# Performance work log

Hardware: AMD Instinct MI355X
Metric: run time of the kernel (lower is better)

The kernel has to match this reference:

```python
import jax, jax.numpy as jnp
import numpy as np

D_MODEL, NUM_HEADS, D_FF = 1024, 16, 4096
HEAD_DIM = D_MODEL // NUM_HEADS
EPS = 1e-5


def _layernorm(x, g, b):
    m = jnp.mean(x, axis=-1, keepdims=True)
    v = jnp.mean((x - m) ** 2, axis=-1, keepdims=True)
    return (x - m) * jax.lax.rsqrt(v + EPS) * g + b


def setup_inputs() -> dict:
    key = jax.random.key(0)
    ks = jax.random.split(key, 16)
    N, S = 4, 2048
    x = jax.random.normal(ks[0], (N, S, D_MODEL), dtype=jnp.float32)
    # mask broadcastable against energy of shape (N, S, H, H) -- see notes: code
    # computes per-position head-vs-head attention, not SxS attention.
    mask = jax.random.randint(ks[1], (N, 1, 1, NUM_HEADS), 0, 2, dtype=jnp.int32)
    s = 0.02
    return {
        "x": x,
        "Wqkv": jax.random.normal(ks[2], (D_MODEL, 3 * D_MODEL), dtype=jnp.float32) * s,
        "bqkv": jnp.zeros((3 * D_MODEL,), jnp.float32),
        "Wo": jax.random.normal(ks[3], (D_MODEL, D_MODEL), dtype=jnp.float32) * s,
        "bo": jnp.zeros((D_MODEL,), jnp.float32),
        "g1": jnp.ones((D_MODEL,), jnp.float32),
        "beta1": jnp.zeros((D_MODEL,), jnp.float32),
        "W1": jax.random.normal(ks[4], (D_MODEL, D_FF), dtype=jnp.float32) * s,
        "bf1": jnp.zeros((D_FF,), jnp.float32),
        "W2": jax.random.normal(ks[5], (D_FF, D_MODEL), dtype=jnp.float32) * s,
        "bf2": jnpp if False else jnp.zeros((D_MODEL,), jnp.float32),
        "g2": jnp.ones((D_MODEL,), jnp.float32),
        "beta2": jnp.zeros((D_MODEL,), jnp.float32),
        "mask": mask,
    }


def reference(x, Wqkv, bqkv, Wo, bo, g1, beta1, W1, bf1, W2, bf2, g2, beta2, mask):
    N, S, D = x.shape
    H, hd = NUM_HEADS, HEAD_DIM
    # fused QKV projection
    qkv = (x @ Wqkv + bqkv).reshape(N, S, 3, H, hd).transpose(2, 0, 3, 1, 4)
    q, k, v = qkv[0], qkv[1], qkv[2]  # each (N, H, S, hd)
    # faithful to torch einsum 'nqhd,nkhd->nhqk' on (N,H,S,hd) operands:
    # energy[n,s,i,j] = sum_d q[n,i,s,d] * k[n,j,s,d]  -> (N, S, H, H)
    energy = jnp.einsum('nise,njse->nsij', q, k)
    energy = jnp.where(mask == 0, jnp.float32(-1e20), energy)
    attn = jax.nn.softmax(energy / np.sqrt(hd).astype(np.float32), axis=3)
    # torch einsum 'nhql,nlhd->nqhd': out[n,i,s,d] = sum_l attn[n,s,i,l]*v[n,l,s,d]
    out = jnp.einsum('nsil,nlse->nise', attn, v)  # (N, H, S, hd)
    out = out.reshape(N, S, D)  # row-major flatten, exactly as torch .reshape
    attn_out = out @ Wo + bo
    h = _layernorm(attn_out + x, g1, beta1)
    ff = jax.nn.relu(h @ W1 + bf1) @ W2 + bf2  # dropout = identity (eval)
    return _layernorm(ff + h, g2, beta2)
```

## Files before the change

### kernel.cpp

```cpp
#include <hip/hip_runtime.h>
#include <cstdint>
#include <cstddef>


using f32x4  = __attribute__((ext_vector_type(4))) float;
using bf16x8 = __attribute__((ext_vector_type(8))) __bf16;

__device__ __forceinline__ unsigned short f2b(float f) {
  union { float f; uint32_t u; } v; v.f = f;
  uint32_t r = v.u + 0x7FFFu + ((v.u >> 16) & 1u);
  return (unsigned short)(r >> 16);
}
__device__ __forceinline__ float b2f(unsigned short u) {
  union { uint32_t u; float f; } v; v.u = ((uint32_t)u) << 16;
  return v.f;
}

__device__ __forceinline__ void gload_lds16(const unsigned short* g,
                                            unsigned short* l) {
  __builtin_amdgcn_global_load_lds(
      (const __attribute__((address_space(1))) unsigned int*)g,
      (__attribute__((address_space(3))) unsigned int*)l, 16, 0, 0);
}

#define MEMBAR() asm volatile("" ::: "memory")
__device__ __forceinline__ void barrier_raw() {
  MEMBAR();
  __builtin_amdgcn_s_barrier();
  MEMBAR();
}
template <int N>
__device__ __forceinline__ void vmwait() {
  if constexpr (N == 6)      asm volatile("s_waitcnt vmcnt(6)" ::: "memory");
  else if constexpr (N == 5) asm volatile("s_waitcnt vmcnt(5)" ::: "memory");
  else                       asm volatile("s_waitcnt vmcnt(0)" ::: "memory");
}

__global__ __launch_bounds__(256) void transpose_cvt_kernel(
    const float* __restrict__ W, unsigned short* __restrict__ WT, int K, int N) {
  __shared__ float tile[32][33];
  const int j0 = blockIdx.x * 32, k0 = blockIdx.y * 32;
  const int tx = threadIdx.x, ty = threadIdx.y;
#pragma unroll
  for (int i = 0; i < 4; ++i)
    tile[ty + 8 * i][tx] = W[(size_t)(k0 + ty + 8 * i) * N + j0 + tx];
  __syncthreads();
#pragma unroll
  for (int i = 0; i < 4; ++i)
    WT[(size_t)(j0 + ty + 8 * i) * K + k0 + tx] = f2b(tile[tx][ty + 8 * i]);
}

__global__ __launch_bounds__(256) void cvt_bf16_kernel(
    const float* __restrict__ in, unsigned short* __restrict__ out, int n4) {
  for (int i = blockIdx.x * blockDim.x + threadIdx.x; i < n4;
       i += gridDim.x * blockDim.x) {
    float4 v = ((const float4*)in)[i];
    uint32_t lo = (uint32_t)f2b(v.x) | ((uint32_t)f2b(v.y) << 16);
    uint32_t hi = (uint32_t)f2b(v.z) | ((uint32_t)f2b(v.w) << 16);
    ((uint2*)out)[i] = make_uint2(lo, hi);
  }
}

template <int BN, bool OUTB, bool RELU>
__global__ __launch_bounds__(512, 2) void gemm8p_kernel(
    const unsigned short* __restrict__ A, const unsigned short* __restrict__ B,
    const float* __restrict__ bias, void* __restrict__ C, int M, int N, int K,
    int nbn) {
  constexpr int NF   = BN / 128;
  constexpr int WN   = BN / 8;
  constexpr int BH   = BN / 2;
  constexpr int BIS  = BN / 128;
  constexpr int INF  = 4 + BN / 128;
  constexpr int ASTR = (256 + BN) * 64;

  __shared__ unsigned short lds[2 * ASTR];

  const int tid  = threadIdx.x;
  const int lane = tid & 63, wave = tid >> 6;
  const int wm = wave >> 2, wn = wave & 3;
  const int lr = lane & 15, lk = lane >> 4;
  const int x7 = lr & 7;

  const int nwg = gridDim.x, cpx = nwg >> 3, id = blockIdx.x;
  const int wg = (id & 7) * cpx + (id >> 3);
  const int bn = wg % nbn, bm = wg / nbn;

  const unsigned short* Ab = A + (size_t)bm * 256 * K;
  const unsigned short* Bb = B + (size_t)bn * BN * K;

  const int srow = tid >> 3;
  const int scol = ((tid & 7) ^ (srow & 7)) * 8;
  const int ldst = wave * 8 * 64;

  const int NT = K >> 6;

  f32x4 acc[8][2 * NF] = {};
  bf16x8 aF[4][2], b0F[NF][2], b1F[NF][2];

  auto stA = [&](int t, int h, int b) {
#pragma unroll
    for (int i = 0; i < 2; ++i)
      gload_lds16(Ab + (size_t)(h * 128 + i * 64 + srow) * K + t * 64 + scol,
                  &lds[b * ASTR + (h * 128 + i * 64) * 64 + ldst]);
  };
  auto stB = [&](int t, int h, int b) {
#pragma unroll
    for (int i = 0; i < BIS; ++i)
      gload_lds16(Bb + (size_t)(h * BH + i * 64 + srow) * K + t * 64 + scol,
                  &lds[b * ASTR + 256 * 64 + (h * BH + i * 64) * 64 + ldst]);
  };
  auto rdA = [&](int b, int mh) {
#pragma unroll
    for (int mi = 0; mi < 4; ++mi) {
      int r = mh * 128 + wm * 64 + mi * 16 + lr;
#pragma unroll
      for (int kk = 0; kk < 2; ++kk)
        aF[mi][kk] = *(const bf16x8*)
            &lds[b * ASTR + r * 64 + ((kk * 4 + lk) ^ x7) * 8];
    }
  };
  auto rdB = [&](int b, int nh, bf16x8 (&bF)[NF][2]) {
#pragma unroll
    for (int ni = 0; ni < NF; ++ni) {
      int r = nh * BH + wn * WN + ni * 16 + lr;
#pragma unroll
      for (int kk = 0; kk < 2; ++kk)
        bF[ni][kk] = *(const bf16x8*)
            &lds[b * ASTR + 256 * 64 + r * 64 + ((kk * 4 + lk) ^ x7) * 8];
    }
  };
  auto mmQ = [&](bf16x8 (&bF)[NF][2], int mh, int nh) {
    __builtin_amdgcn_s_setprio(1);
#pragma unroll
    for (int mi = 0; mi < 4; ++mi)
#pragma unroll
      for (int ni = 0; ni < NF; ++ni)
#pragma unroll
        for (int kk = 0; kk < 2; ++kk)
          acc[mh * 4 + mi][nh * NF + ni] = __builtin_amdgcn_mfma_f32_16x16x32_bf16(
              aF[mi][kk], bF[ni][kk], acc[mh * 4 + mi][nh * NF + ni], 0, 0, 0);
    __builtin_amdgcn_s_setprio(0);
  };

  stA(0, 0, 0); stB(0, 0, 0); stA(0, 1, 0); stB(0, 1, 0);
  stA(1, 0, 1); stB(1, 0, 1); stA(1, 1, 1);
  vmwait<INF>();
  barrier_raw();

  for (int t = 0; t < NT; ++t) {
    const int b = t & 1;
    const bool s1 = (t + 1 < NT), s2 = (t + 2 < NT);
    rdA(b, 0);
    rdB(b, 0, b0F);
    if (s1) stB(t + 1, 1, b ^ 1);
    barrier_raw();
    mmQ(b0F, 0, 0);
    barrier_raw();
    rdB(b, 1, b1F);
    if (s2) stA(t + 2, 0, b);
    barrier_raw();
    mmQ(b1F, 0, 1);
    barrier_raw();
    rdA(b, 1);
    if (s2) stB(t + 2, 0, b);
    barrier_raw();
    mmQ(b1F, 1, 1);
    barrier_raw();
    if (s2) {
      stA(t + 2, 1, b);
      vmwait<INF>();
    } else if (s1) {
      vmwait<0>();
    }
    barrier_raw();
    mmQ(b0F, 1, 0);
    barrier_raw();
  }

  const int orow0 = bm * 256 + wm * 64;
  const int ocol0 = bn * BN + wn * WN;
#pragma unroll
  for (int mh = 0; mh < 2; ++mh)
#pragma unroll
    for (int nh = 0; nh < 2; ++nh)
#pragma unroll
      for (int ni = 0; ni < NF; ++ni) {
        int col = ocol0 + nh * BH + ni * 16 + lr;
        float bv = bias[col];
#pragma unroll
        for (int mi = 0; mi < 4; ++mi)
#pragma unroll
          for (int r = 0; r < 4; ++r) {
            int row = orow0 + mh * 128 + mi * 16 + lk * 4 + r;
            float val = acc[mh * 4 + mi][nh * NF + ni][r] + bv;
            if (RELU) val = fmaxf(val, 0.f);
            if (OUTB)
              ((unsigned short*)C)[(size_t)row * N + col] = f2b(val);
            else
              ((float*)C)[(size_t)row * N + col] = val;
          }
      }
}

__global__ __launch_bounds__(256) void attn_kernel(
    const unsigned short* __restrict__ qkv, const int* __restrict__ mask,
    unsigned short* __restrict__ outb) {
  __shared__ float sq[16][68], sk[16][68], sv[16][68];
  __shared__ float sp[16][17];
  const int pos = blockIdx.x;
  const int n = pos >> 11, s = pos & 2047;
  const int tid = threadIdx.x;
  const unsigned short* row = qkv + (size_t)pos * 3072;
#pragma unroll
  for (int it = 0; it < 3; ++it) {
    uint2 raw = *(const uint2*)(row + it * 1024 + tid * 4);
    float f0 = b2f((unsigned short)(raw.x & 0xffffu));
    float f1 = b2f((unsigned short)(raw.x >> 16));
    float f2 = b2f((unsigned short)(raw.y & 0xffffu));
    float f3 = b2f((unsigned short)(raw.y >> 16));
    float(*dst)[68] = (it == 0) ? sq : (it == 1) ? sk : sv;
    int r = tid >> 4, d = (tid & 15) * 4;
    dst[r][d] = f0; dst[r][d + 1] = f1; dst[r][d + 2] = f2; dst[r][d + 3] = f3;
  }
  __syncthreads();
  {
    const int i = tid >> 4, j = tid & 15;
    float e = 0.f;
#pragma unroll
    for (int d = 0; d < 64; d += 4) {
      float4 qa = *(const float4*)&sq[i][d];
      float4 kb = *(const float4*)&sk[j][d];
      e += qa.x * kb.x + qa.y * kb.y + qa.z * kb.z + qa.w * kb.w;
    }
    if (mask[n * 16 + j] == 0) e = -1e20f;
    e *= 0.125f;
    float mx = e;
#pragma unroll
    for (int o = 8; o > 0; o >>= 1) mx = fmaxf(mx, __shfl_xor(mx, o, 16));
    float pe = __expf(e - mx);
    float sm = pe;
#pragma unroll
    for (int o = 8; o > 0; o >>= 1) sm += __shfl_xor(sm, o, 16);
    sp[i][j] = pe / sm;
  }
  __syncthreads();
  {
    const int w = tid >> 6, d = tid & 63;
    float o0 = 0, o1 = 0, o2 = 0, o3 = 0;
#pragma unroll
    for (int l = 0; l < 16; ++l) {
      float vv = sv[l][d];
      o0 += sp[w][l] * vv;      o1 += sp[w + 4][l] * vv;
      o2 += sp[w + 8][l] * vv;  o3 += sp[w + 12][l] * vv;
    }
    outb[(((size_t)n * 16 + w     ) * 2048 + s) * 64 + d] = f2b(o0);
    outb[(((size_t)n * 16 + w + 4 ) * 2048 + s) * 64 + d] = f2b(o1);
    outb[(((size_t)n * 16 + w + 8 ) * 2048 + s) * 64 + d] = f2b(o2);
    outb[(((size_t)n * 16 + w + 12) * 2048 + s) * 64 + d] = f2b(o3);
  }
}

__global__ __launch_bounds__(256) void ln_kernel(
    const float* __restrict__ A, const float* __restrict__ R,
    const float* __restrict__ g, const float* __restrict__ be,
    float* __restrict__ outf, unsigned short* __restrict__ outb) {
  const int row = blockIdx.x, tid = threadIdx.x;
  const size_t base = (size_t)row * 1024 + tid * 4;
  float4 a = *(const float4*)(A + base);
  float4 r = *(const float4*)(R + base);
  float x0 = a.x + r.x, x1 = a.y + r.y, x2 = a.z + r.z, x3 = a.w + r.w;
  float s = x0 + x1 + x2 + x3;
#pragma unroll
  for (int o = 32; o > 0; o >>= 1) s += __shfl_xor(s, o);
  __shared__ float red[4];
  const int lane = tid & 63, wv = tid >> 6;
  if (lane == 0) red[wv] = s;
  __syncthreads();
  float mean = (red[0] + red[1] + red[2] + red[3]) * (1.f / 1024.f);
  float d0 = x0 - mean, d1 = x1 - mean, d2 = x2 - mean, d3 = x3 - mean;
  float q = d0 * d0 + d1 * d1 + d2 * d2 + d3 * d3;
#pragma unroll
  for (int o = 32; o > 0; o >>= 1) q += __shfl_xor(q, o);
  __syncthreads();
  if (lane == 0) red[wv] = q;
  __syncthreads();
  float var = (red[0] + red[1] + red[2] + red[3]) * (1.f / 1024.f);
  float rs = rsqrtf(var + 1e-5f);
  const int col = tid * 4;
  float4 gv = *(const float4*)(g + col);
  float4 bv = *(const float4*)(be + col);
  float y0 = d0 * rs * gv.x + bv.x;
  float y1 = d1 * rs * gv.y + bv.y;
  float y2 = d2 * rs * gv.z + bv.z;
  float y3 = d3 * rs * gv.w + bv.w;
  *(float4*)(outf + base) = make_float4(y0, y1, y2, y3);
  if (outb) {
    uint32_t lo = (uint32_t)f2b(y0) | ((uint32_t)f2b(y1) << 16);
    uint32_t hi = (uint32_t)f2b(y2) | ((uint32_t)f2b(y3) << 16);
    *(uint2*)(outb + base) = make_uint2(lo, hi);
  }
}

extern "C" void kernel_launch(void* const* d_in, const int* in_sizes, int n_in,
                              void* d_out, int out_size, void* d_ws,
                              size_t ws_size, hipStream_t stream) {
  (void)in_sizes; (void)n_in; (void)out_size; (void)ws_size;
  const float* x     = (const float*)d_in[0];
  const float* Wqkv  = (const float*)d_in[1];
  const float* bqkv  = (const float*)d_in[2];
  const float* Wo    = (const float*)d_in[3];
  const float* bo    = (const float*)d_in[4];
  const float* g1    = (const float*)d_in[5];
  const float* beta1 = (const float*)d_in[6];
  const float* W1    = (const float*)d_in[7];
  const float* bf1   = (const float*)d_in[8];
  const float* W2    = (const float*)d_in[9];
  const float* bf2   = (const float*)d_in[10];
  const float* g2    = (const float*)d_in[11];
  const float* beta2 = (const float*)d_in[12];
  const int*   mask  = (const int*)d_in[13];
  float* out = (float*)d_out;

  char* ws = (char*)d_ws;
  unsigned short* WqkvT = (unsigned short*)(ws + 0);
  unsigned short* WoT   = (unsigned short*)(ws + 6291456);
  unsigned short* W1T   = (unsigned short*)(ws + 8388608);
  unsigned short* W2T   = (unsigned short*)(ws + 16777216);
  unsigned short* xb    = (unsigned short*)(ws + 25165824);
  float*          h_f   = (float*)(ws + 41943040);
  unsigned short* h_b   = (unsigned short*)(ws + 75497472);
  float*          ao2   = (float*)(ws + 92274688);
  unsigned short* qkvb  = (unsigned short*)(ws + 125829120);
  unsigned short* aob   = (unsigned short*)(ws + 176160768);
  unsigned short* ff1   = qkvb;
  float*          ff2   = ao2;

  transpose_cvt_kernel<<<dim3(96, 32),  dim3(32, 8), 0, stream>>>(Wqkv, WqkvT, 1024, 3072);
  transpose_cvt_kernel<<<dim3(32, 32),  dim3(32, 8), 0, stream>>>(Wo,   WoT,   1024, 1024);
  transpose_cvt_kernel<<<dim3(128, 32), dim3(32, 8), 0, stream>>>(W1,   W1T,   1024, 4096);
  transpose_cvt_kernel<<<dim3(32, 128), dim3(32, 8), 0, stream>>>(W2,   W2T,   4096, 1024);
  cvt_bf16_kernel<<<2048, 256, 0, stream>>>(x, xb, 8192 * 1024 / 4);

  gemm8p_kernel<256, true, false><<<dim3(32 * 12), 512, 0, stream>>>(xb, WqkvT, bqkv, qkvb, 8192, 3072, 1024, 12);
  attn_kernel<<<8192, 256, 0, stream>>>(qkvb, mask, aob);
  gemm8p_kernel<128, false, false><<<dim3(32 * 8), 512, 0, stream>>>(aob, WoT, bo, ao2, 8192, 1024, 1024, 8);
  ln_kernel<<<8192, 256, 0, stream>>>(ao2, x, g1, beta1, h_f, h_b);
  gemm8p_kernel<256, true, true><<<dim3(32 * 16), 512, 0, stream>>>(h_b, W1T, bf1, ff1, 8192, 4096, 1024, 16);
  gemm8p_kernel<128, false, false><<<dim3(32 * 8), 512, 0, stream>>>(ff1, W2T, bf2, ff2, 8192, 1024, 4096, 8);
  ln_kernel<<<8192, 256, 0, stream>>>(ff2, h_f, g2, beta2, out, nullptr);
}
```

Measured before the change: 329.8 us.

## Use split-K with wider tiles for FFN2 GEMM and merge partials in LayerNorm

Measured after the change: 329.8 us. No clear change (+0.0%).

```diff
diff --git a/kernel.cpp b/kernel.cpp
--- a/kernel.cpp
+++ b/kernel.cpp
@@ -61,11 +61,11 @@
   }
 }
 
-template <int BN, bool OUTB, bool RELU>
+template <int BN, bool SPLITK, bool OUTB, bool RELU>
 __global__ __launch_bounds__(512, 2) void gemm8p_kernel(
     const unsigned short* __restrict__ A, const unsigned short* __restrict__ B,
-    const float* __restrict__ bias, void* __restrict__ C, int M, int N, int K,
-    int nbn) {
+    const float* __restrict__ bias, void* __restrict__ C,
+    unsigned short* __restrict__ C2, int M, int N, int Ks, int Kd, int nbn) {
   constexpr int NF   = BN / 128;
   constexpr int WN   = BN / 8;
   constexpr int BH   = BN / 2;
@@ -83,16 +83,18 @@
 
   const int nwg = gridDim.x, cpx = nwg >> 3, id = blockIdx.x;
   const int wg = (id & 7) * cpx + (id >> 3);
-  const int bn = wg % nbn, bm = wg / nbn;
-
-  const unsigned short* Ab = A + (size_t)bm * 256 * K;
-  const unsigned short* Bb = B + (size_t)bn * BN * K;
+  int bm, bn, sk;
+  if (SPLITK) { bm = wg >> 3; bn = (wg & 7) >> 1; sk = wg & 1; }
+  else        { bm = wg / nbn; bn = wg % nbn; sk = 0; }
+
+  const unsigned short* Ab = A + (size_t)bm * 256 * Ks + (size_t)sk * Kd;
+  const unsigned short* Bb = B + (size_t)bn * BN * Ks + (size_t)sk * Kd;
 
   const int srow = tid >> 3;
   const int scol = ((tid & 7) ^ (srow & 7)) * 8;
   const int ldst = wave * 8 * 64;
 
-  const int NT = K >> 6;
+  const int NT = Kd >> 6;
 
   f32x4 acc[8][2 * NF] = {};
   bf16x8 aF[4][2], b0F[NF][2], b1F[NF][2];
@@ -100,13 +102,13 @@
   auto stA = [&](int t, int h, int b) {
 #pragma unroll
     for (int i = 0; i < 2; ++i)
-      gload_lds16(Ab + (size_t)(h * 128 + i * 64 + srow) * K + t * 64 + scol,
+      gload_lds16(Ab + (size_t)(h * 128 + i * 64 + srow) * Ks + t * 64 + scol,
                   &lds[b * ASTR + (h * 128 + i * 64) * 64 + ldst]);
   };
   auto stB = [&](int t, int h, int b) {
 #pragma unroll
     for (int i = 0; i < BIS; ++i)
-      gload_lds16(Bb + (size_t)(h * BH + i * 64 + srow) * K + t * 64 + scol,
+      gload_lds16(Bb + (size_t)(h * BH + i * 64 + srow) * Ks + t * 64 + scol,
                   &lds[b * ASTR + 256 * 64 + (h * BH + i * 64) * 64 + ldst]);
   };
   auto rdA = [&](int b, int mh) {
@@ -192,12 +194,20 @@
 #pragma unroll
           for (int r = 0; r < 4; ++r) {
             int row = orow0 + mh * 128 + mi * 16 + lk * 4 + r;
-            float val = acc[mh * 4 + mi][nh * NF + ni][r] + bv;
-            if (RELU) val = fmaxf(val, 0.f);
-            if (OUTB)
-              ((unsigned short*)C)[(size_t)row * N + col] = f2b(val);
-            else
-              ((float*)C)[(size_t)row * N + col] = val;
+            float val = acc[mh * 4 + mi][nh * NF + ni][r];
+            if (SPLITK) {
+              if (sk == 0)
+                ((float*)C)[(size_t)row * N + col] = val + bv;
+              else
+                C2[(size_t)row * N + col] = f2b(val);
+            } else {
+              val += bv;
+              if (RELU) val = fmaxf(val, 0.f);
+              if (OUTB)
+                ((unsigned short*)C)[(size_t)row * N + col] = f2b(val);
+              else
+                ((float*)C)[(size_t)row * N + col] = val;
+            }
           }
       }
 }
@@ -261,7 +271,8 @@
 }
 
 __global__ __launch_bounds__(256) void ln_kernel(
-    const float* __restrict__ A, const float* __restrict__ R,
+    const float* __restrict__ A, const unsigned short* __restrict__ P2,
+    const float* __restrict__ R,
     const float* __restrict__ g, const float* __restrict__ be,
     float* __restrict__ outf, unsigned short* __restrict__ outb) {
   const int row = blockIdx.x, tid = threadIdx.x;
@@ -269,6 +280,13 @@
   float4 a = *(const float4*)(A + base);
   float4 r = *(const float4*)(R + base);
   float x0 = a.x + r.x, x1 = a.y + r.y, x2 = a.z + r.z, x3 = a.w + r.w;
+  if (P2) {
+    uint2 p = *(const uint2*)(P2 + base);
+    x0 += b2f((unsigned short)(p.x & 0xffffu));
+    x1 += b2f((unsigned short)(p.x >> 16));
+    x2 += b2f((unsigned short)(p.y & 0xffffu));
+    x3 += b2f((unsigned short)(p.y >> 16));
+  }
   float s = x0 + x1 + x2 + x3;
 #pragma unroll
   for (int o = 32; o > 0; o >>= 1) s += __shfl_xor(s, o);
@@ -334,6 +352,7 @@
   unsigned short* aob   = (unsigned short*)(ws + 176160768);
   unsigned short* ff1   = qkvb;
   float*          ff2   = ao2;
+  unsigned short* ff2p2 = xb;
 
   transpose_cvt_kernel<<<dim3(96, 32),  dim3(32, 8), 0, stream>>>(Wqkv, WqkvT, 1024, 3072);
   transpose_cvt_kernel<<<dim3(32, 32),  dim3(32, 8), 0, stream>>>(Wo,   WoT,   1024, 1024);
@@ -341,11 +360,15 @@
   transpose_cvt_kernel<<<dim3(32, 128), dim3(32, 8), 0, stream>>>(W2,   W2T,   4096, 1024);
   cvt_bf16_kernel<<<2048, 256, 0, stream>>>(x, xb, 8192 * 1024 / 4);
 
-  gemm8p_kernel<256, true, false><<<dim3(32 * 12), 512, 0, stream>>>(xb, WqkvT, bqkv, qkvb, 8192, 3072, 1024, 12);
+  gemm8p_kernel<256, false, true, false><<<dim3(32 * 12), 512, 0, stream>>>(
+      xb, WqkvT, bqkv, qkvb, nullptr, 8192, 3072, 1024, 1024, 12);
   attn_kernel<<<8192, 256, 0, stream>>>(qkvb, mask, aob);
-  gemm8p_kernel<128, false, false><<<dim3(32 * 8), 512, 0, stream>>>(aob, WoT, bo, ao2, 8192, 1024, 1024, 8);
-  ln_kernel<<<8192, 256, 0, stream>>>(ao2, x, g1, beta1, h_f, h_b);
-  gemm8p_kernel<256, true, true><<<dim3(32 * 16), 512, 0, stream>>>(h_b, W1T, bf1, ff1, 8192, 4096, 1024, 16);
-  gemm8p_kernel<128, false, false><<<dim3(32 * 8), 512, 0, stream>>>(ff1, W2T, bf2, ff2, 8192, 1024, 4096, 8);
-  ln_kernel<<<8192, 256, 0, stream>>>(ff2, h_f, g2, beta2, out, nullptr);
-}
+  gemm8p_kernel<128, false, false, false><<<dim3(32 * 8), 512, 0, stream>>>(
+      aob, WoT, bo, ao2, nullptr, 8192, 1024, 1024, 1024, 8);
+  ln_kernel<<<8192, 256, 0, stream>>>(ao2, nullptr, x, g1, beta1, h_f, h_b);
+  gemm8p_kernel<256, false, true, true><<<dim3(32 * 16), 512, 0, stream>>>(
+      h_b, W1T, bf1, ff1, nullptr, 8192, 4096, 1024, 1024, 16);
+  gemm8p_kernel<256, true, false, false><<<dim3(32 * 8), 512, 0, stream>>>(
+      ff1, W2T, bf2, ff2, ff2p2, 8192, 1024, 4096, 2048, 4);
+  ln_kernel<<<8192, 256, 0, stream>>>(ff2, ff2p2, h_f, g2, beta2, out, nullptr);
+}
```
